# Optimization experiments

Hardware: AMD Instinct MI355X
Metric: run time of the kernel (lower is better)

Reference implementation:

```python
import jax, jax.numpy as jnp
import numpy as np
import math

B, N, C = 32, 576, 1024
INNER, H = 256, 4
HD = INNER // H
ALPHA = 5.0
EPS = 1e-5

def _layer_norm(x, w, b):
    mu = jnp.mean(x, axis=-1, keepdims=True)
    var = jnp.mean((x - mu) ** 2, axis=-1, keepdims=True)
    return (x - mu) * jax.lax.rsqrt(var + EPS) * w + b

def setup_inputs() -> dict:
    key = jax.random.key(0)
    ks = jax.random.split(key, 20)
    def lin(k, out_d, in_d):
        scale = math.sqrt(6.0 / (in_d + out_d))
        return jax.random.uniform(k, (out_d, in_d), jnp.float32, -scale, scale)
    return {
        'query_features': jax.random.normal(ks[0], (B, N, C), jnp.float32),
        'support_features': jax.random.normal(ks[1], (B, N, C), jnp.float32),
        'support_mask_weights': jax.random.uniform(ks[2], (B, N), jnp.float32),
        'ln_q_w': jnp.ones((C,), jnp.float32), 'ln_q_b': jnp.zeros((C,), jnp.float32),
        'ln_s_w': jnp.ones((C,), jnp.float32), 'ln_s_b': jnp.zeros((C,), jnp.float32),
        'Wq': lin(ks[3], INNER, C), 'bq': jnp.zeros((INNER,), jnp.float32),
        'Wk': lin(ks[4], INNER, C), 'bk': jnp.zeros((INNER,), jnp.float32),
        'Wv': lin(ks[5], INNER, C), 'bv': jnp.zeros((INNER,), jnp.float32),
        'Wo': lin(ks[6], C, INNER), 'bo': jnp.zeros((C,), jnp.float32),
        'Wg': 0.02 * jax.random.normal(ks[7], (C, C), jnp.float32),
        'bg': jnp.full((C,), -1.0, jnp.float32),
    }

def reference(query_features, support_features, support_mask_weights,
              ln_q_w, ln_q_b, ln_s_w, ln_s_b,
              Wq, bq, Wk, bk, Wv, bv, Wo, bo, Wg, bg):
    q = _layer_norm(query_features, ln_q_w, ln_q_b)
    s = _layer_norm(support_features, ln_s_w, ln_s_b)
    Q = (q @ Wq.T + bq).reshape(B, N, H, HD).transpose(0, 2, 1, 3)  # (B,H,N,HD)
    K = (s @ Wk.T + bk).reshape(B, N, H, HD).transpose(0, 2, 1, 3)
    V = (s @ Wv.T + bv).reshape(B, N, H, HD).transpose(0, 2, 1, 3)
    logits = jnp.einsum('bhnd,bhmd->bhnm', Q, K) / math.sqrt(HD)
    logits = logits + ALPHA * support_mask_weights[:, None, None, :]
    attn = jax.nn.softmax(logits, axis=-1)
    ctx = jnp.einsum('bhnm,bhmd->bhnd', attn, V).transpose(0, 2, 1, 3).reshape(B, N, INNER)
    out = ctx @ Wo.T + bo
    gate = jax.nn.sigmoid(query_features @ Wg.T + bg)
    enhanced = query_features + gate * out
    return enhanced, attn
```

## Files before the change

kernel.cpp:

```cpp
#include <hip/hip_runtime.h>
#include <hip/hip_bf16.h>
#include <math.h>

#define B_ 32
#define N_ 576
#define C_ 1024
#define INNER_ 256
#define H_ 4
#define HD_ 64
#define M_ (B_*N_)
#define ALPHA_ 5.0f
#define EPS_ 1e-5f

typedef __attribute__((ext_vector_type(8))) short bf16x8;
typedef __attribute__((ext_vector_type(4))) float f32x4;
typedef __attribute__((ext_vector_type(4))) unsigned int u32x4;
typedef unsigned short u16;

__device__ inline u16 bfbits(float x) {
    union { __hip_bfloat16 h; u16 u; } c; c.h = __float2bfloat16(x); return c.u;
}
__device__ inline unsigned pack2bf(float a, float b) {
    return (unsigned)bfbits(a) | ((unsigned)bfbits(b) << 16);
}

template<int GX, int GY>
__device__ inline void xcd_remap(int& col, int& row) {
    int f = blockIdx.y * GX + blockIdx.x;
    int xcd = f & 7;
    int slot = f >> 3;
    col = slot % GX;
    row = xcd * (GY >> 3) + slot / GX;
}

__global__ void ln_fused2_kernel(const float* __restrict__ Xq, const float* __restrict__ Xs,
                                 const float* __restrict__ wq, const float* __restrict__ bq,
                                 const float* __restrict__ ws, const float* __restrict__ bs,
                                 u16* __restrict__ outq, u16* __restrict__ outs) {
    const float* X; const float* w; const float* b; u16* o;
    if (blockIdx.y == 0) { X = Xq; w = wq; b = bq; o = outq; }
    else                 { X = Xs; w = ws; b = bs; o = outs; }
    int row = blockIdx.x * 4 + (threadIdx.x >> 6);
    int lane = threadIdx.x & 63;
    const float* xp = X + (size_t)row * C_;
    float4 v[4];
    #pragma unroll
    for (int j = 0; j < 4; ++j) v[j] = *(const float4*)(xp + lane*4 + j*256);
    float s = 0.f, s2 = 0.f;
    #pragma unroll
    for (int j = 0; j < 4; ++j) {
        s  += v[j].x + v[j].y + v[j].z + v[j].w;
        s2 += v[j].x*v[j].x + v[j].y*v[j].y + v[j].z*v[j].z + v[j].w*v[j].w;
    }
    #pragma unroll
    for (int m = 32; m; m >>= 1) {
        s  += __shfl_xor(s,  m, 64);
        s2 += __shfl_xor(s2, m, 64);
    }
    float mean = s * (1.f/C_);
    float rs = rsqrtf(s2 * (1.f/C_) - mean*mean + EPS_);
    #pragma unroll
    for (int j = 0; j < 4; ++j) {
        int k = lane*4 + j*256;
        float4 wv = *(const float4*)(w + k);
        float4 bv = *(const float4*)(b + k);
        ushort4 ov;
        ov.x = bfbits((v[j].x - mean)*rs*wv.x + bv.x);
        ov.y = bfbits((v[j].y - mean)*rs*wv.y + bv.y);
        ov.z = bfbits((v[j].z - mean)*rs*wv.z + bv.z);
        ov.w = bfbits((v[j].w - mean)*rs*wv.w + bv.w);
        *(ushort4*)(o + (size_t)row*C_ + k) = ov;
    }
}

__global__ void cvt_weights_kernel(const float* __restrict__ Wq, const float* __restrict__ Wk,
                                   const float* __restrict__ Wv, const float* __restrict__ Wo,
                                   const float* __restrict__ Wg,
                                   const float* __restrict__ bk, const float* __restrict__ bv,
                                   u16* __restrict__ Wq_b, u16* __restrict__ Wkv_b,
                                   u16* __restrict__ Wo_b, u16* __restrict__ Wg_b,
                                   float* __restrict__ bkv) {
    if (blockIdx.x == 0 && threadIdx.x < 128) {
        float4 t = (threadIdx.x < 64) ? ((const float4*)bk)[threadIdx.x]
                                      : ((const float4*)bv)[threadIdx.x - 64];
        ((float4*)bkv)[threadIdx.x] = t;
    }
    int g = blockIdx.x * 256 + threadIdx.x;
    const float* src; u16* dst; size_t off;
    if (g < 32768)       { src = Wq; dst = Wq_b;          off = (size_t)g*8; }
    else if (g < 65536)  { src = Wk; dst = Wkv_b;         off = (size_t)(g-32768)*8; }
    else if (g < 98304)  { src = Wv; dst = Wkv_b + 262144; off = (size_t)(g-65536)*8; }
    else if (g < 131072) { src = Wo; dst = Wo_b;          off = (size_t)(g-98304)*8; }
    else                 { src = Wg; dst = Wg_b;          off = (size_t)(g-131072)*8; }
    float4 a0 = *(const float4*)(src + off);
    float4 a1 = *(const float4*)(src + off + 4);
    union { u16 s[8]; u32x4 v; } o;
    o.s[0] = bfbits(a0.x); o.s[1] = bfbits(a0.y); o.s[2] = bfbits(a0.z); o.s[3] = bfbits(a0.w);
    o.s[4] = bfbits(a1.x); o.s[5] = bfbits(a1.y); o.s[6] = bfbits(a1.z); o.s[7] = bfbits(a1.w);
    *(u32x4*)(dst + off) = o.v;
}

template<int KDIM, bool F32A>
__device__ inline void gemm_accum(const void* __restrict__ Ap, const u16* __restrict__ Bw,
                                  int row0, int col0, int tid, int lane, int wm, int wn,
                                  u16 (&Asm)[128][72], u16 (&Bsm)[128][72],
                                  f32x4 (&acc)[4][4]) {
    for (int k0 = 0; k0 < KDIM; k0 += 64) {
        #pragma unroll
        for (int i = 0; i < 4; ++i) {
            int s = tid + i*256;
            int r = s >> 3, cg = (s & 7) * 8;
            u32x4 vb = *(const u32x4*)(Bw + (size_t)(col0 + r)*KDIM + k0 + cg);
            if (F32A) {
                const float* a = (const float*)Ap + (size_t)(row0 + r)*KDIM + k0 + cg;
                float4 a0 = *(const float4*)a;
                float4 a1 = *(const float4*)(a + 4);
                union { u16 s[8]; u32x4 v; } o;
                o.s[0]=bfbits(a0.x); o.s[1]=bfbits(a0.y); o.s[2]=bfbits(a0.z); o.s[3]=bfbits(a0.w);
                o.s[4]=bfbits(a1.x); o.s[5]=bfbits(a1.y); o.s[6]=bfbits(a1.z); o.s[7]=bfbits(a1.w);
                *(u32x4*)&Asm[r][cg] = o.v;
            } else {
                *(u32x4*)&Asm[r][cg] =
                    *(const u32x4*)((const u16*)Ap + (size_t)(row0 + r)*KDIM + k0 + cg);
            }
            *(u32x4*)&Bsm[r][cg] = vb;
        }
        __syncthreads();
        #pragma unroll
        for (int ks = 0; ks < 64; ks += 32) {
            bf16x8 af[4], bfr[4];
            #pragma unroll
            for (int i = 0; i < 4; ++i)
                af[i] = *(const bf16x8*)&Asm[wm + i*16 + (lane & 15)][ks + (lane >> 4)*8];
            #pragma unroll
            for (int j = 0; j < 4; ++j)
                bfr[j] = *(const bf16x8*)&Bsm[wn + j*16 + (lane & 15)][ks + (lane >> 4)*8];
            #pragma unroll
            for (int i = 0; i < 4; ++i)
                #pragma unroll
                for (int j = 0; j < 4; ++j)
                    acc[i][j] = __builtin_amdgcn_mfma_f32_16x16x32_bf16(
                        af[i], bfr[j], acc[i][j], 0, 0, 0);
        }
        __syncthreads();
    }
}

__global__ __launch_bounds__(256, 2)
void qkv_gemm_kernel(const u16* __restrict__ Aq, const u16* __restrict__ As,
                     const u16* __restrict__ Wq_b, const u16* __restrict__ Wkv_b,
                     const float* __restrict__ bq, const float* __restrict__ bkv,
                     u16* __restrict__ Qbf, u16* __restrict__ KVbf) {
    __shared__ u16 Asm[128][72];
    __shared__ u16 Bsm[128][72];
    int tid = threadIdx.x;
    int lane = tid & 63, wid = tid >> 6;
    int wm = (wid >> 1) * 64, wn = (wid & 1) * 64;
    int bc, br;
    xcd_remap<6, 144>(bc, br);
    int row0 = br * 128;
    bool isQ = (bc < 2);
    int col0 = (isQ ? bc : bc - 2) * 128;
    const u16* A  = isQ ? Aq   : As;
    const u16* Bw = isQ ? Wq_b : Wkv_b;
    const float* bias = isQ ? bq : bkv;
    u16* Out = isQ ? Qbf : KVbf;
    const int NOUT = isQ ? INNER_ : 2*INNER_;
    f32x4 acc[4][4] = {};
    gemm_accum<C_, false>(A, Bw, row0, col0, tid, lane, wm, wn, Asm, Bsm, acc);
    #pragma unroll
    for (int i = 0; i < 4; ++i) {
        #pragma unroll
        for (int j = 0; j < 4; ++j) {
            int col = col0 + wn + j*16 + (lane & 15);
            float bb = bias[col];
            #pragma unroll
            for (int r = 0; r < 4; ++r) {
                int row = row0 + wm + i*16 + (lane >> 4)*4 + r;
                Out[(size_t)row * NOUT + col] = bfbits(acc[i][j][r] + bb);
            }
        }
    }
}

__global__ __launch_bounds__(256, 2)
void final_fused_kernel(const float* __restrict__ query,
                        const u16* __restrict__ Wg_b, const float* __restrict__ bg,
                        const u16* __restrict__ ctxb, const u16* __restrict__ Wo_b,
                        const float* __restrict__ bo, float* __restrict__ out) {
    __shared__ u16 Asm[128][72];
    __shared__ u16 Bsm[128][72];
    int tid = threadIdx.x;
    int lane = tid & 63, wid = tid >> 6;
    int wm = (wid >> 1) * 64, wn = (wid & 1) * 64;
    int bc, br;
    xcd_remap<8, 144>(bc, br);
    int row0 = br * 128, col0 = bc * 128;
    f32x4 acc_o[4][4] = {};
    f32x4 acc_g[4][4] = {};
    gemm_accum<INNER_, false>(ctxb, Wo_b, row0, col0, tid, lane, wm, wn, Asm, Bsm, acc_o);
    gemm_accum<C_, true>(query, Wg_b, row0, col0, tid, lane, wm, wn, Asm, Bsm, acc_g);
    #pragma unroll
    for (int i = 0; i < 4; ++i) {
        #pragma unroll
        for (int j = 0; j < 4; ++j) {
            int col = col0 + wn + j*16 + (lane & 15);
            float bgv = bg[col], bov = bo[col];
            #pragma unroll
            for (int r = 0; r < 4; ++r) {
                int row = row0 + wm + i*16 + (lane >> 4)*4 + r;
                size_t idx = (size_t)row * C_ + col;
                float g = 1.f / (1.f + expf(-(acc_g[i][j][r] + bgv)));
                __builtin_nontemporal_store(query[idx] + g * (acc_o[i][j][r] + bov), &out[idx]);
            }
        }
    }
}

__device__ inline void stage_v_half(const u16* __restrict__ KV, u16* __restrict__ Vt,
                                    int b, int h, int HF, int tid) {
    #pragma unroll
    for (int i = 0; i < 9; ++i) {
        int c = tid + i*256;
        int k = c >> 3;
        int d0 = (c & 7) * 8;
        union { u32x4 v; u16 s[8]; } u;
        u.v = *(const u32x4*)(KV + ((size_t)(b*N_ + HF*288 + k))*512 + 256 + h*HD_ + d0);
        #pragma unroll
        for (int e = 0; e < 8; ++e)
            Vt[(d0 + e)*296 + k] = u.s[e];
    }
}

template<int HF>
__device__ inline void pv_half(const unsigned (&pk)[36][2], f32x4 (&cacc)[4],
                               const u16* __restrict__ Vt, int lane) {
    int s1 = (lane & 15) + ((lane & 16) << 1);
    int s2 = s1 + 16;
    bool hi = (lane & 32) != 0;
    #pragma unroll
    for (int t9 = 0; t9 < 9; ++t9) {
        const int t = HF*9 + t9;
        unsigned A01 = __shfl((int)pk[2*t  ][0], s1, 64);
        unsigned A23 = __shfl((int)pk[2*t  ][1], s1, 64);
        unsigned B01 = __shfl((int)pk[2*t+1][0], s1, 64);
        unsigned B23 = __shfl((int)pk[2*t+1][1], s1, 64);
        unsigned C01 = __shfl((int)pk[2*t  ][0], s2, 64);
        unsigned C23 = __shfl((int)pk[2*t  ][1], s2, 64);
        unsigned D01 = __shfl((int)pk[2*t+1][0], s2, 64);
        unsigned D23 = __shfl((int)pk[2*t+1][1], s2, 64);
        union { unsigned w[4]; bf16x8 v; } bu;
        bu.w[0] = hi ? B01 : A01;
        bu.w[1] = hi ? B23 : A23;
        bu.w[2] = hi ? D01 : C01;
        bu.w[3] = hi ? D23 : C23;
        int colb = 32*t - 288*HF + 8*(lane >> 4);
        #pragma unroll
        for (int dt = 0; dt < 4; ++dt) {
            bf16x8 a = *(const bf16x8*)&Vt[(16*dt + (lane & 15))*296 + colb];
            cacc[dt] = __builtin_amdgcn_mfma_f32_16x16x32_bf16(a, bu.v, cacc[dt], 0, 0, 0);
        }
    }
}

__global__ __launch_bounds__(256, 2)
void attn_mfma_kernel(const u16* __restrict__ Qbf, const u16* __restrict__ KV,
                      const float* __restrict__ mask,
                      float* __restrict__ attn_out, u16* __restrict__ ctxb) {
    __shared__ u16 Vt[64*296];
    __shared__ float Msk[576];
    int tid = threadIdx.x;
    int lane = tid & 63, wid = tid >> 6;
    int qb, bh;
    xcd_remap<9, 128>(qb, bh);
    int b = bh >> 2, h = bh & 3;
    int q0 = qb * 64;
    int g = lane >> 4;
    int qrow = q0 + wid*16 + (lane & 15);

    if (tid < 144) {
        float4 mv = *(const float4*)(mask + b*N_ + tid*4);
        *(float4*)&Msk[tid*4] = make_float4(ALPHA_*mv.x, ALPHA_*mv.y, ALPHA_*mv.z, ALPHA_*mv.w);
    }
    stage_v_half(KV, Vt, b, h, 0, tid);
    __syncthreads();

    const u16* qp = Qbf + ((size_t)(b*N_) + qrow)*INNER_ + h*HD_ + g*8;
    bf16x8 qf0 = *(const bf16x8*)qp;
    bf16x8 qf1 = *(const bf16x8*)(qp + 32);

    f32x4 acc[36];
    #pragma unroll
    for (int T = 0; T < 36; ++T) acc[T] = (f32x4){0.f, 0.f, 0.f, 0.f};

    const u16* kp = KV + ((size_t)(b*N_) + (lane & 15))*512 + h*HD_ + g*8;
    bf16x8 kb[2][2];
    kb[0][0] = *(const bf16x8*)(kp);
    kb[0][1] = *(const bf16x8*)(kp + 32);
    kb[1][0] = *(const bf16x8*)(kp + 16*512);
    kb[1][1] = *(const bf16x8*)(kp + 16*512 + 32);
    #pragma unroll
    for (int T = 0; T < 36; ++T) {
        bf16x8 n0, n1;
        if (T + 2 < 36) {
            n0 = *(const bf16x8*)(kp + (size_t)(T+2)*16*512);
            n1 = *(const bf16x8*)(kp + (size_t)(T+2)*16*512 + 32);
        }
        acc[T] = __builtin_amdgcn_mfma_f32_16x16x32_bf16(kb[T&1][0], qf0, acc[T], 0, 0, 0);
        acc[T] = __builtin_amdgcn_mfma_f32_16x16x32_bf16(kb[T&1][1], qf1, acc[T], 0, 0, 0);
        if (T + 2 < 36) { kb[T&1][0] = n0; kb[T&1][1] = n1; }
    }

    float m = -1e30f;
    #pragma unroll
    for (int T = 0; T < 36; ++T) {
        float4 mk = *(const float4*)&Msk[16*T + 4*g];
        acc[T][0] = acc[T][0]*0.125f + mk.x;
        acc[T][1] = acc[T][1]*0.125f + mk.y;
        acc[T][2] = acc[T][2]*0.125f + mk.z;
        acc[T][3] = acc[T][3]*0.125f + mk.w;
        m = fmaxf(m, fmaxf(fmaxf(acc[T][0], acc[T][1]), fmaxf(acc[T][2], acc[T][3])));
    }
    m = fmaxf(m, __shfl_xor(m, 16, 64));
    m = fmaxf(m, __shfl_xor(m, 32, 64));

    float l = 0.f;
    #pragma unroll
    for (int T = 0; T < 36; ++T) {
        acc[T][0] = expf(acc[T][0] - m);
        acc[T][1] = expf(acc[T][1] - m);
        acc[T][2] = expf(acc[T][2] - m);
        acc[T][3] = expf(acc[T][3] - m);
        l += acc[T][0] + acc[T][1] + acc[T][2] + acc[T][3];
    }
    l += __shfl_xor(l, 16, 64);
    l += __shfl_xor(l, 32, 64);
    float inv = 1.f / l;

    unsigned pk[36][2];
    float* ap = attn_out + ((size_t)bh*N_ + qrow)*N_;
    #pragma unroll
    for (int T = 0; T < 36; ++T) {
        float e0 = acc[T][0]*inv, e1 = acc[T][1]*inv;
        float e2 = acc[T][2]*inv, e3 = acc[T][3]*inv;
        f32x4 ov = {e0, e1, e2, e3};
        __builtin_nontemporal_store(ov, (f32x4*)(ap + 16*T + 4*g));
        pk[T][0] = pack2bf(e0, e1);
        pk[T][1] = pack2bf(e2, e3);
    }

    f32x4 cacc[4] = {};
    pv_half<0>(pk, cacc, Vt, lane);
    __syncthreads();
    stage_v_half(KV, Vt, b, h, 1, tid);
    __syncthreads();
    pv_half<1>(pk, cacc, Vt, lane);

    u16* cp = ctxb + ((size_t)(b*N_) + qrow)*INNER_ + h*HD_ + 4*g;
    #pragma unroll
    for (int dt = 0; dt < 4; ++dt) {
        ushort4 o;
        o.x = bfbits(cacc[dt][0]);
        o.y = bfbits(cacc[dt][1]);
        o.z = bfbits(cacc[dt][2]);
        o.w = bfbits(cacc[dt][3]);
        *(ushort4*)(cp + 16*dt) = o;
    }
}

extern "C" void kernel_launch(void* const* d_in, const int* in_sizes, int n_in,
                              void* d_out, int out_size, void* d_ws, size_t ws_size,
                              hipStream_t stream) {
    const float* query   = (const float*)d_in[0];
    const float* support = (const float*)d_in[1];
    const float* mask    = (const float*)d_in[2];
    const float* ln_q_w  = (const float*)d_in[3];
    const float* ln_q_b  = (const float*)d_in[4];
    const float* ln_s_w  = (const float*)d_in[5];
    const float* ln_s_b  = (const float*)d_in[6];
    const float* Wq      = (const float*)d_in[7];
    const float* bq      = (const float*)d_in[8];
    const float* Wk      = (const float*)d_in[9];
    const float* bk      = (const float*)d_in[10];
    const float* Wv      = (const float*)d_in[11];
    const float* bv      = (const float*)d_in[12];
    const float* Wo      = (const float*)d_in[13];
    const float* bo      = (const float*)d_in[14];
    const float* Wg      = (const float*)d_in[15];
    const float* bg      = (const float*)d_in[16];

    float* out      = (float*)d_out;
    float* attn_out = out + (size_t)M_ * C_;

    char* w = (char*)d_ws;
    u16* Aq    = (u16*)w;  w += (size_t)M_*C_*2;
    u16* As_   = (u16*)w;  w += (size_t)M_*C_*2;
    u16* Wq_b  = (u16*)w;  w += (size_t)INNER_*C_*2;
    u16* Wkv_b = (u16*)w;  w += (size_t)2*INNER_*C_*2;
    u16* Wo_b  = (u16*)w;  w += (size_t)C_*INNER_*2;
    u16* Wg_b  = (u16*)w;  w += (size_t)C_*C_*2;
    float* bkv = (float*)w; w += 512*4;
    u16* Qbf   = (u16*)w;  w += (size_t)M_*INNER_*2;
    u16* KVbf  = (u16*)w;  w += (size_t)M_*2*INNER_*2;
    u16* ctxb  = (u16*)w;  w += (size_t)M_*INNER_*2;

    ln_fused2_kernel<<<dim3(M_/4, 2), dim3(256), 0, stream>>>(
        query, support, ln_q_w, ln_q_b, ln_s_w, ln_s_b, Aq, As_);

    cvt_weights_kernel<<<dim3(1024), dim3(256), 0, stream>>>(
        Wq, Wk, Wv, Wo, Wg, bk, bv, Wq_b, Wkv_b, Wo_b, Wg_b, bkv);

    qkv_gemm_kernel<<<dim3(6, 144), dim3(256), 0, stream>>>(
        Aq, As_, Wq_b, Wkv_b, bq, bkv, Qbf, KVbf);

    attn_mfma_kernel<<<dim3(N_/64, B_*H_), dim3(256), 0, stream>>>(
        Qbf, KVbf, mask, attn_out, ctxb);

    final_fused_kernel<<<dim3(8, 144), dim3(256), 0, stream>>>(
        query, Wg_b, bg, ctxb, Wo_b, bo, out);
}
```

Measured before the change: 307.9 us.

## Use direct global-to-LDS loads in GEMMs and precompute bf16 query copy

```diff
diff --git a/kernel.cpp b/kernel.cpp
--- a/kernel.cpp
+++ b/kernel.cpp
@@ -24,6 +24,12 @@
     return (unsigned)bfbits(a) | ((unsigned)bfbits(b) << 16);
 }
 
+__device__ __forceinline__ void gld16(void* lds, const void* g) {
+    __builtin_amdgcn_global_load_lds(
+        (const __attribute__((address_space(1))) unsigned int*)g,
+        (__attribute__((address_space(3))) unsigned int*)lds, 16, 0, 0);
+}
+
 template<int GX, int GY>
 __device__ inline void xcd_remap(int& col, int& row) {
     int f = blockIdx.y * GX + blockIdx.x;
@@ -36,10 +42,12 @@
 __global__ void ln_fused2_kernel(const float* __restrict__ Xq, const float* __restrict__ Xs,
                                  const float* __restrict__ wq, const float* __restrict__ bq,
                                  const float* __restrict__ ws, const float* __restrict__ bs,
-                                 u16* __restrict__ outq, u16* __restrict__ outs) {
+                                 u16* __restrict__ outq, u16* __restrict__ outs,
+                                 u16* __restrict__ outraw) {
     const float* X; const float* w; const float* b; u16* o;
-    if (blockIdx.y == 0) { X = Xq; w = wq; b = bq; o = outq; }
-    else                 { X = Xs; w = ws; b = bs; o = outs; }
+    bool raw = (blockIdx.y == 0);
+    if (raw) { X = Xq; w = wq; b = bq; o = outq; }
+    else     { X = Xs; w = ws; b = bs; o = outs; }
     int row = blockIdx.x * 4 + (threadIdx.x >> 6);
     int lane = threadIdx.x & 63;
     const float* xp = X + (size_t)row * C_;
@@ -70,6 +78,12 @@
         ov.z = bfbits((v[j].z - mean)*rs*wv.z + bv.z);
         ov.w = bfbits((v[j].w - mean)*rs*wv.w + bv.w);
         *(ushort4*)(o + (size_t)row*C_ + k) = ov;
+        if (raw) {
+            ushort4 r4;
+            r4.x = bfbits(v[j].x); r4.y = bfbits(v[j].y);
+            r4.z = bfbits(v[j].z); r4.w = bfbits(v[j].w);
+            *(ushort4*)(outraw + (size_t)row*C_ + k) = r4;
+        }
     }
 }
 
@@ -100,30 +114,22 @@
     *(u32x4*)(dst + off) = o.v;
 }
 
-template<int KDIM, bool F32A>
-__device__ inline void gemm_accum(const void* __restrict__ Ap, const u16* __restrict__ Bw,
-                                  int row0, int col0, int tid, int lane, int wm, int wn,
-                                  u16 (&Asm)[128][72], u16 (&Bsm)[128][72],
-                                  f32x4 (&acc)[4][4]) {
+template<int KDIM>
+__device__ __forceinline__ void gemm_accum_async(const u16* __restrict__ A,
+                                                 const u16* __restrict__ Bw,
+                                                 int row0, int col0, int tid, int lane,
+                                                 int wm, int wn,
+                                                 u16 (&Asm)[128][64], u16 (&Bsm)[128][64],
+                                                 f32x4 (&acc)[4][4]) {
+    int rb = tid >> 3, cg = (tid & 7) * 8;
     for (int k0 = 0; k0 < KDIM; k0 += 64) {
         #pragma unroll
-        for (int i = 0; i < 4; ++i) {
-            int s = tid + i*256;
-            int r = s >> 3, cg = (s & 7) * 8;
-            u32x4 vb = *(const u32x4*)(Bw + (size_t)(col0 + r)*KDIM + k0 + cg);
-            if (F32A) {
-                const float* a = (const float*)Ap + (size_t)(row0 + r)*KDIM + k0 + cg;
-                float4 a0 = *(const float4*)a;
-                float4 a1 = *(const float4*)(a + 4);
-                union { u16 s[8]; u32x4 v; } o;
-                o.s[0]=bfbits(a0.x); o.s[1]=bfbits(a0.y); o.s[2]=bfbits(a0.z); o.s[3]=bfbits(a0.w);
-                o.s[4]=bfbits(a1.x); o.s[5]=bfbits(a1.y); o.s[6]=bfbits(a1.z); o.s[7]=bfbits(a1.w);
-                *(u32x4*)&Asm[r][cg] = o.v;
-            } else {
-                *(u32x4*)&Asm[r][cg] =
-                    *(const u32x4*)((const u16*)Ap + (size_t)(row0 + r)*KDIM + k0 + cg);
-            }
-            *(u32x4*)&Bsm[r][cg] = vb;
+        for (int p = 0; p < 4; ++p) {
+            int rr = p*32 + rb;
+            gld16(&Asm[0][0] + ((size_t)(p*256 + tid))*8,
+                  A + (size_t)(row0 + rr)*KDIM + k0 + cg);
+            gld16(&Bsm[0][0] + ((size_t)(p*256 + tid))*8,
+                  Bw + (size_t)(col0 + rr)*KDIM + k0 + cg);
         }
         __syncthreads();
         #pragma unroll
@@ -146,13 +152,13 @@
     }
 }
 
-__global__ __launch_bounds__(256, 2)
+__global__ __launch_bounds__(256, 4)
 void qkv_gemm_kernel(const u16* __restrict__ Aq, const u16* __restrict__ As,
                      const u16* __restrict__ Wq_b, const u16* __restrict__ Wkv_b,
                      const float* __restrict__ bq, const float* __restrict__ bkv,
                      u16* __restrict__ Qbf, u16* __restrict__ KVbf) {
-    __shared__ u16 Asm[128][72];
-    __shared__ u16 Bsm[128][72];
+    __shared__ u16 Asm[128][64];
+    __shared__ u16 Bsm[128][64];
     int tid = threadIdx.x;
     int lane = tid & 63, wid = tid >> 6;
     int wm = (wid >> 1) * 64, wn = (wid & 1) * 64;
@@ -167,7 +173,7 @@
     u16* Out = isQ ? Qbf : KVbf;
     const int NOUT = isQ ? INNER_ : 2*INNER_;
     f32x4 acc[4][4] = {};
-    gemm_accum<C_, false>(A, Bw, row0, col0, tid, lane, wm, wn, Asm, Bsm, acc);
+    gemm_accum_async<C_>(A, Bw, row0, col0, tid, lane, wm, wn, Asm, Bsm, acc);
     #pragma unroll
     for (int i = 0; i < 4; ++i) {
         #pragma unroll
@@ -183,13 +189,13 @@
     }
 }
 
-__global__ __launch_bounds__(256, 2)
-void final_fused_kernel(const float* __restrict__ query,
+__global__ __launch_bounds__(256, 3)
+void final_fused_kernel(const float* __restrict__ query, const u16* __restrict__ Xq,
                         const u16* __restrict__ Wg_b, const float* __restrict__ bg,
                         const u16* __restrict__ ctxb, const u16* __restrict__ Wo_b,
                         const float* __restrict__ bo, float* __restrict__ out) {
-    __shared__ u16 Asm[128][72];
-    __shared__ u16 Bsm[128][72];
+    __shared__ u16 Asm[128][64];
+    __shared__ u16 Bsm[128][64];
     int tid = threadIdx.x;
     int lane = tid & 63, wid = tid >> 6;
     int wm = (wid >> 1) * 64, wn = (wid & 1) * 64;
@@ -198,8 +204,8 @@
     int row0 = br * 128, col0 = bc * 128;
     f32x4 acc_o[4][4] = {};
     f32x4 acc_g[4][4] = {};
-    gemm_accum<INNER_, false>(ctxb, Wo_b, row0, col0, tid, lane, wm, wn, Asm, Bsm, acc_o);
-    gemm_accum<C_, true>(query, Wg_b, row0, col0, tid, lane, wm, wn, Asm, Bsm, acc_g);
+    gemm_accum_async<INNER_>(ctxb, Wo_b, row0, col0, tid, lane, wm, wn, Asm, Bsm, acc_o);
+    gemm_accum_async<C_>(Xq, Wg_b, row0, col0, tid, lane, wm, wn, Asm, Bsm, acc_g);
     #pragma unroll
     for (int i = 0; i < 4; ++i) {
         #pragma unroll
@@ -395,6 +401,7 @@
     char* w = (char*)d_ws;
     u16* Aq    = (u16*)w;  w += (size_t)M_*C_*2;
     u16* As_   = (u16*)w;  w += (size_t)M_*C_*2;
+    u16* Xq    = (u16*)w;  w += (size_t)M_*C_*2;
     u16* Wq_b  = (u16*)w;  w += (size_t)INNER_*C_*2;
     u16* Wkv_b = (u16*)w;  w += (size_t)2*INNER_*C_*2;
     u16* Wo_b  = (u16*)w;  w += (size_t)C_*INNER_*2;
@@ -405,7 +412,7 @@
     u16* ctxb  = (u16*)w;  w += (size_t)M_*INNER_*2;
 
     ln_fused2_kernel<<<dim3(M_/4, 2), dim3(256), 0, stream>>>(
-        query, support, ln_q_w, ln_q_b, ln_s_w, ln_s_b, Aq, As_);
+        query, support, ln_q_w, ln_q_b, ln_s_w, ln_s_b, Aq, As_, Xq);
 
     cvt_weights_kernel<<<dim3(1024), dim3(256), 0, stream>>>(
         Wq, Wk, Wv, Wo, Wg, bk, bv, Wq_b, Wkv_b, Wo_b, Wg_b, bkv);
@@ -417,5 +424,5 @@
         Qbf, KVbf, mask, attn_out, ctxb);
 
     final_fused_kernel<<<dim3(8, 144), dim3(256), 0, stream>>>(
-        query, Wg_b, bg, ctxb, Wo_b, bo, out);
-}
+        query, Xq, Wg_b, bg, ctxb, Wo_b, bo, out);
+}
```

Measured after the change: 324.2 us. +5.3%, slower.

## Split gate GEMM from output projection to reduce register pressure

Applied to the files above, without the earlier changes.

```diff
diff --git a/kernel.cpp b/kernel.cpp
--- a/kernel.cpp
+++ b/kernel.cpp
@@ -19,6 +19,9 @@
 
 __device__ inline u16 bfbits(float x) {
     union { __hip_bfloat16 h; u16 u; } c; c.h = __float2bfloat16(x); return c.u;
+}
+__device__ inline float bf2f(u16 u) {
+    union { unsigned u32; float f; } c; c.u32 = ((unsigned)u) << 16; return c.f;
 }
 __device__ inline unsigned pack2bf(float a, float b) {
     return (unsigned)bfbits(a) | ((unsigned)bfbits(b) << 16);
@@ -146,7 +149,7 @@
     }
 }
 
-__global__ __launch_bounds__(256, 2)
+__global__ __launch_bounds__(256, 4)
 void qkv_gemm_kernel(const u16* __restrict__ Aq, const u16* __restrict__ As,
                      const u16* __restrict__ Wq_b, const u16* __restrict__ Wkv_b,
                      const float* __restrict__ bq, const float* __restrict__ bkv,
@@ -183,11 +186,9 @@
     }
 }
 
-__global__ __launch_bounds__(256, 2)
-void final_fused_kernel(const float* __restrict__ query,
-                        const u16* __restrict__ Wg_b, const float* __restrict__ bg,
-                        const u16* __restrict__ ctxb, const u16* __restrict__ Wo_b,
-                        const float* __restrict__ bo, float* __restrict__ out) {
+__global__ __launch_bounds__(256, 4)
+void gate_gemm_kernel(const float* __restrict__ query, const u16* __restrict__ Wg_b,
+                      const float* __restrict__ bg, u16* __restrict__ Gbf) {
     __shared__ u16 Asm[128][72];
     __shared__ u16 Bsm[128][72];
     int tid = threadIdx.x;
@@ -196,22 +197,50 @@
     int bc, br;
     xcd_remap<8, 144>(bc, br);
     int row0 = br * 128, col0 = bc * 128;
-    f32x4 acc_o[4][4] = {};
-    f32x4 acc_g[4][4] = {};
-    gemm_accum<INNER_, false>(ctxb, Wo_b, row0, col0, tid, lane, wm, wn, Asm, Bsm, acc_o);
-    gemm_accum<C_, true>(query, Wg_b, row0, col0, tid, lane, wm, wn, Asm, Bsm, acc_g);
+    f32x4 acc[4][4] = {};
+    gemm_accum<C_, true>(query, Wg_b, row0, col0, tid, lane, wm, wn, Asm, Bsm, acc);
     #pragma unroll
     for (int i = 0; i < 4; ++i) {
         #pragma unroll
         for (int j = 0; j < 4; ++j) {
             int col = col0 + wn + j*16 + (lane & 15);
-            float bgv = bg[col], bov = bo[col];
+            float bb = bg[col];
+            #pragma unroll
+            for (int r = 0; r < 4; ++r) {
+                int row = row0 + wm + i*16 + (lane >> 4)*4 + r;
+                float v = acc[i][j][r] + bb;
+                Gbf[(size_t)row*C_ + col] = bfbits(1.f / (1.f + expf(-v)));
+            }
+        }
+    }
+}
+
+__global__ __launch_bounds__(256, 4)
+void final_lite_kernel(const float* __restrict__ query, const u16* __restrict__ Gbf,
+                       const u16* __restrict__ ctxb, const u16* __restrict__ Wo_b,
+                       const float* __restrict__ bo, float* __restrict__ out) {
+    __shared__ u16 Asm[128][72];
+    __shared__ u16 Bsm[128][72];
+    int tid = threadIdx.x;
+    int lane = tid & 63, wid = tid >> 6;
+    int wm = (wid >> 1) * 64, wn = (wid & 1) * 64;
+    int bc, br;
+    xcd_remap<8, 144>(bc, br);
+    int row0 = br * 128, col0 = bc * 128;
+    f32x4 acc[4][4] = {};
+    gemm_accum<INNER_, false>(ctxb, Wo_b, row0, col0, tid, lane, wm, wn, Asm, Bsm, acc);
+    #pragma unroll
+    for (int i = 0; i < 4; ++i) {
+        #pragma unroll
+        for (int j = 0; j < 4; ++j) {
+            int col = col0 + wn + j*16 + (lane & 15);
+            float bov = bo[col];
             #pragma unroll
             for (int r = 0; r < 4; ++r) {
                 int row = row0 + wm + i*16 + (lane >> 4)*4 + r;
                 size_t idx = (size_t)row * C_ + col;
-                float g = 1.f / (1.f + expf(-(acc_g[i][j][r] + bgv)));
-                __builtin_nontemporal_store(query[idx] + g * (acc_o[i][j][r] + bov), &out[idx]);
+                float g = bf2f(Gbf[idx]);
+                __builtin_nontemporal_store(query[idx] + g * (acc[i][j][r] + bov), &out[idx]);
             }
         }
     }
@@ -403,6 +432,7 @@
     u16* Qbf   = (u16*)w;  w += (size_t)M_*INNER_*2;
     u16* KVbf  = (u16*)w;  w += (size_t)M_*2*INNER_*2;
     u16* ctxb  = (u16*)w;  w += (size_t)M_*INNER_*2;
+    u16* Gbf   = Aq;
 
     ln_fused2_kernel<<<dim3(M_/4, 2), dim3(256), 0, stream>>>(
         query, support, ln_q_w, ln_q_b, ln_s_w, ln_s_b, Aq, As_);
@@ -416,6 +446,9 @@
     attn_mfma_kernel<<<dim3(N_/64, B_*H_), dim3(256), 0, stream>>>(
         Qbf, KVbf, mask, attn_out, ctxb);
 
-    final_fused_kernel<<<dim3(8, 144), dim3(256), 0, stream>>>(
-        query, Wg_b, bg, ctxb, Wo_b, bo, out);
-}
+    gate_gemm_kernel<<<dim3(8, 144), dim3(256), 0, stream>>>(
+        query, Wg_b, bg, Gbf);
+
+    final_lite_kernel<<<dim3(8, 144), dim3(256), 0, stream>>>(
+        query, Gbf, ctxb, Wo_b, bo, out);
+}
```

New measurement: 372.4 us. +20.9%, slower.

## Split final kernel into gate and output-projection warp groups within 512-thread block

Applied to the files above, without the earlier changes.

```diff
diff --git a/kernel.cpp b/kernel.cpp
--- a/kernel.cpp
+++ b/kernel.cpp
@@ -19,6 +19,9 @@
 
 __device__ inline u16 bfbits(float x) {
     union { __hip_bfloat16 h; u16 u; } c; c.h = __float2bfloat16(x); return c.u;
+}
+__device__ inline float bf2f(u16 u) {
+    union { unsigned u32; float f; } c; c.u32 = ((unsigned)u) << 16; return c.f;
 }
 __device__ inline unsigned pack2bf(float a, float b) {
     return (unsigned)bfbits(a) | ((unsigned)bfbits(b) << 16);
@@ -183,35 +186,111 @@
     }
 }
 
-__global__ __launch_bounds__(256, 2)
-void final_fused_kernel(const float* __restrict__ query,
+__global__ __launch_bounds__(512, 4)
+void final_split_kernel(const float* __restrict__ query,
                         const u16* __restrict__ Wg_b, const float* __restrict__ bg,
                         const u16* __restrict__ ctxb, const u16* __restrict__ Wo_b,
                         const float* __restrict__ bo, float* __restrict__ out) {
-    __shared__ u16 Asm[128][72];
-    __shared__ u16 Bsm[128][72];
+    __shared__ __align__(16) char ldsraw[73728];
+    u16 (*AsmO)[72] = (u16(*)[72])(ldsraw);
+    u16 (*BsmO)[72] = (u16(*)[72])(ldsraw + 18432);
+    u16 (*AsmG)[72] = (u16(*)[72])(ldsraw + 36864);
+    u16 (*BsmG)[72] = (u16(*)[72])(ldsraw + 55296);
+    u16* gateLds = (u16*)(ldsraw + 36864);
+
     int tid = threadIdx.x;
-    int lane = tid & 63, wid = tid >> 6;
+    bool isG = (tid >= 256);
+    int gtid = tid & 255;
+    int lane = gtid & 63, wid = gtid >> 6;
     int wm = (wid >> 1) * 64, wn = (wid & 1) * 64;
     int bc, br;
     xcd_remap<8, 144>(bc, br);
     int row0 = br * 128, col0 = bc * 128;
-    f32x4 acc_o[4][4] = {};
-    f32x4 acc_g[4][4] = {};
-    gemm_accum<INNER_, false>(ctxb, Wo_b, row0, col0, tid, lane, wm, wn, Asm, Bsm, acc_o);
-    gemm_accum<C_, true>(query, Wg_b, row0, col0, tid, lane, wm, wn, Asm, Bsm, acc_g);
-    #pragma unroll
-    for (int i = 0; i < 4; ++i) {
-        #pragma unroll
-        for (int j = 0; j < 4; ++j) {
-            int col = col0 + wn + j*16 + (lane & 15);
-            float bgv = bg[col], bov = bo[col];
-            #pragma unroll
-            for (int r = 0; r < 4; ++r) {
-                int row = row0 + wm + i*16 + (lane >> 4)*4 + r;
-                size_t idx = (size_t)row * C_ + col;
-                float g = 1.f / (1.f + expf(-(acc_g[i][j][r] + bgv)));
-                __builtin_nontemporal_store(query[idx] + g * (acc_o[i][j][r] + bov), &out[idx]);
+
+    u16 (*Asm)[72] = isG ? AsmG : AsmO;
+    u16 (*Bsm)[72] = isG ? BsmG : BsmO;
+    const int KD = isG ? C_ : INNER_;
+    const u16* Bw = isG ? Wg_b : Wo_b;
+
+    f32x4 acc[4][4] = {};
+    int sr = gtid >> 3, scg = (gtid & 7) * 8;
+
+    for (int step = 0; step < 16; ++step) {
+        bool active = isG || (step < 4);
+        if (active) {
+            int k0 = step * 64;
+            #pragma unroll
+            for (int i = 0; i < 4; ++i) {
+                int r = sr + i*32;
+                if (isG) {
+                    const float* a = query + (size_t)(row0 + r)*C_ + k0 + scg;
+                    float4 a0 = *(const float4*)a;
+                    float4 a1 = *(const float4*)(a + 4);
+                    union { u16 s[8]; u32x4 v; } o;
+                    o.s[0]=bfbits(a0.x); o.s[1]=bfbits(a0.y); o.s[2]=bfbits(a0.z); o.s[3]=bfbits(a0.w);
+                    o.s[4]=bfbits(a1.x); o.s[5]=bfbits(a1.y); o.s[6]=bfbits(a1.z); o.s[7]=bfbits(a1.w);
+                    *(u32x4*)&Asm[r][scg] = o.v;
+                } else {
+                    *(u32x4*)&Asm[r][scg] =
+                        *(const u32x4*)(ctxb + (size_t)(row0 + r)*KD + k0 + scg);
+                }
+                *(u32x4*)&Bsm[r][scg] = *(const u32x4*)(Bw + (size_t)(col0 + r)*KD + k0 + scg);
+            }
+        }
+        __syncthreads();
+        if (active) {
+            #pragma unroll
+            for (int ks = 0; ks < 64; ks += 32) {
+                bf16x8 af[4], bfr[4];
+                #pragma unroll
+                for (int i = 0; i < 4; ++i)
+                    af[i] = *(const bf16x8*)&Asm[wm + i*16 + (lane & 15)][ks + (lane >> 4)*8];
+                #pragma unroll
+                for (int j = 0; j < 4; ++j)
+                    bfr[j] = *(const bf16x8*)&Bsm[wn + j*16 + (lane & 15)][ks + (lane >> 4)*8];
+                #pragma unroll
+                for (int i = 0; i < 4; ++i)
+                    #pragma unroll
+                    for (int j = 0; j < 4; ++j)
+                        acc[i][j] = __builtin_amdgcn_mfma_f32_16x16x32_bf16(
+                            af[i], bfr[j], acc[i][j], 0, 0, 0);
+            }
+        }
+        __syncthreads();
+    }
+
+    if (isG) {
+        #pragma unroll
+        for (int i = 0; i < 4; ++i) {
+            #pragma unroll
+            for (int j = 0; j < 4; ++j) {
+                int cl = wn + j*16 + (lane & 15);
+                float bb = bg[col0 + cl];
+                #pragma unroll
+                for (int r = 0; r < 4; ++r) {
+                    int rl = wm + i*16 + (lane >> 4)*4 + r;
+                    float v = acc[i][j][r] + bb;
+                    gateLds[rl*128 + cl] = bfbits(1.f / (1.f + expf(-v)));
+                }
+            }
+        }
+    }
+    __syncthreads();
+
+    if (!isG) {
+        #pragma unroll
+        for (int i = 0; i < 4; ++i) {
+            #pragma unroll
+            for (int j = 0; j < 4; ++j) {
+                int cl = wn + j*16 + (lane & 15);
+                float bov = bo[col0 + cl];
+                #pragma unroll
+                for (int r = 0; r < 4; ++r) {
+                    int rl = wm + i*16 + (lane >> 4)*4 + r;
+                    size_t idx = (size_t)(row0 + rl) * C_ + col0 + cl;
+                    float g = bf2f(gateLds[rl*128 + cl]);
+                    __builtin_nontemporal_store(query[idx] + g * (acc[i][j][r] + bov), &out[idx]);
+                }
             }
         }
     }
@@ -416,6 +495,6 @@
     attn_mfma_kernel<<<dim3(N_/64, B_*H_), dim3(256), 0, stream>>>(
         Qbf, KVbf, mask, attn_out, ctxb);
 
-    final_fused_kernel<<<dim3(8, 144), dim3(256), 0, stream>>>(
+    final_split_kernel<<<dim3(8, 144), dim3(512), 0, stream>>>(
         query, Wg_b, bg, ctxb, Wo_b, bo, out);
 }
```

Result: slower. 396.4 us (+28.7%).
